# Optimization experiments

Measured on AMD Instinct MI355X. Metric: run time of the kernel, lower is better.

Reference implementation:

```python
import jax, jax.numpy as jnp
import numpy as np

MOVING_AVG_RATE = 0.999
EPS_NORM = 1e-12   # F.normalize eps
EPS_MEAN = 1e-6    # cluster mean denom eps


def _l2norm(a):
    n = jnp.linalg.norm(a, axis=1, keepdims=True)
    return a / jnp.maximum(n, EPS_NORM)


def setup_inputs() -> dict:
    key = jax.random.key(0)
    k1, k2 = jax.random.split(key)
    x = jax.random.normal(k1, (8, 512, 64, 64), dtype=jnp.float32)
    m = jax.random.normal(k2, (1024, 512), dtype=jnp.float32)  # codebook [k, c]
    return {"x": x, "m": m}


def reference(x, m):
    b, c, h, w = x.shape
    k = m.shape[0]
    # flatten spatial/batch dims -> tokens [N, c]
    xf = jnp.transpose(x, (0, 2, 3, 1)).reshape(-1, c)
    xn = _l2norm(xf)
    mn = _l2norm(m)
    score = xn @ mn.T  # [N, k] cosine similarity

    # EMA codebook update: hard assignment via argmax, scatter-reduce means
    idx = jnp.argmax(score, axis=1)  # [N]
    counts = jax.ops.segment_sum(jnp.ones(xf.shape[0], dtype=xf.dtype), idx, num_segments=k)
    esum = jax.ops.segment_sum(xf, idx, num_segments=k)  # [k, c]
    emean = esum / (counts[:, None] + EPS_MEAN)
    new_m = m * MOVING_AVG_RATE + emean * (1.0 - MOVING_AVG_RATE)

    # soft combine against the UPDATED codebook
    soft = jax.nn.softmax(score, axis=1)
    out = soft @ new_m  # [N, c]
    return jnp.transpose(out.reshape(b, h, w, c), (0, 3, 1, 2))
```

## Files before the change

### kernel.cpp

```cpp
#include <hip/hip_runtime.h>
#include <hip/hip_bf16.h>
#include <math.h>

#define B 8
#define C 512
#define H 64
#define W 64
#define N 32768
#define K 1024
#define HW 4096
#define CHW 2097152

typedef unsigned short u16;
typedef __attribute__((ext_vector_type(4))) float f32x4;
typedef __attribute__((ext_vector_type(8))) short bf16x8;

#define MNB_OFF   0
#define IDX_OFF   (MNB_OFF + K*C/2)
#define CNT_OFF   (IDX_OFF + N)
#define ESUM_OFF  (CNT_OFF + K)
#define NMT_OFF   (ESUM_OFF + K*C)
#define SCORE_OFF (NMT_OFF + K*C/2)

static __device__ __forceinline__ u16 f2bf(float f) {
    unsigned int u = __float_as_uint(f);
    u += 0x7fffu + ((u >> 16) & 1u);
    return (u16)(u >> 16);
}
static __device__ __forceinline__ float bf2f(unsigned int us) {
    return __uint_as_float(us << 16);
}
static __device__ __forceinline__ unsigned int pack2(float lo, float hi) {
    return (unsigned int)f2bf(lo) | ((unsigned int)f2bf(hi) << 16);
}

static __device__ __forceinline__ void gload_lds16(const void* g, void* l) {
    __builtin_amdgcn_global_load_lds(
        (const __attribute__((address_space(1))) unsigned int*)g,
        (__attribute__((address_space(3))) unsigned int*)l, 16, 0, 0);
}

__global__ void k_norm_mb(const float* __restrict__ m, u16* __restrict__ mnb) {
    int j = blockIdx.x;
    int lane = threadIdx.x;
    const float4* mr = (const float4*)(m + (size_t)j * C);
    float4 a = mr[lane * 2], b = mr[lane * 2 + 1];
    float ss = a.x*a.x + a.y*a.y + a.z*a.z + a.w*a.w
             + b.x*b.x + b.y*b.y + b.z*b.z + b.w*b.w;
#pragma unroll
    for (int o = 32; o >= 1; o >>= 1) ss += __shfl_xor(ss, o);
    float inv = 1.0f / fmaxf(sqrtf(ss), 1e-12f);
    uint4 pk;
    pk.x = pack2(a.x * inv, a.y * inv);
    pk.y = pack2(a.z * inv, a.w * inv);
    pk.z = pack2(b.x * inv, b.y * inv);
    pk.w = pack2(b.z * inv, b.w * inv);
    *(uint4*)(mnb + (size_t)j * C + lane * 8) = pk;
}

__global__ void __launch_bounds__(256) k_prep_x(const float* __restrict__ x,
                                                u16* __restrict__ xb) {
    int bh = blockIdx.x;
    int b = bh >> 6, h = bh & 63;
    int w  = threadIdx.x & 63;
    int wq = threadIdx.x >> 6;
    const float* base = x + (size_t)b * CHW + (size_t)h * W + w;
    float ss = 0.0f;
    for (int ch = wq * 128; ch < wq * 128 + 128; ++ch) {
        float v = base[(size_t)ch * HW];
        ss += v * v;
    }
    __shared__ float red[4][64];
    red[wq][w] = ss;
    __syncthreads();
    float tot = red[0][w] + red[1][w] + red[2][w] + red[3][w];
    float inv = 1.0f / fmaxf(sqrtf(tot), 1e-12f);
    size_t n = (size_t)bh * 64 + w;
    u16* orow = xb + n * C;
    for (int c8 = wq * 128; c8 < wq * 128 + 128; c8 += 8) {
        float v0 = base[(size_t)(c8+0)*HW] * inv;
        float v1 = base[(size_t)(c8+1)*HW] * inv;
        float v2 = base[(size_t)(c8+2)*HW] * inv;
        float v3 = base[(size_t)(c8+3)*HW] * inv;
        float v4 = base[(size_t)(c8+4)*HW] * inv;
        float v5 = base[(size_t)(c8+5)*HW] * inv;
        float v6 = base[(size_t)(c8+6)*HW] * inv;
        float v7 = base[(size_t)(c8+7)*HW] * inv;
        uint4 pk;
        pk.x = pack2(v0, v1); pk.y = pack2(v2, v3);
        pk.z = pack2(v4, v5); pk.w = pack2(v6, v7);
        *(uint4*)&orow[c8] = pk;
    }
}

__global__ void __launch_bounds__(256) k_score_mfma(
        const u16* __restrict__ xb, const u16* __restrict__ mnb,
        u16* __restrict__ score) {
    __shared__ u16 As[128 * 64];
    __shared__ u16 Bs[128 * 64];
    int tid = threadIdx.x;
    int lane = tid & 63;
    int wid = tid >> 6;
    int wm = wid >> 1, wn = wid & 1;
    int n0 = blockIdx.x * 128;
    int j0 = blockIdx.y * 128;

    f32x4 acc[4][4] = {};

    const u16* a_src = xb + (size_t)(n0 + wid*32 + (lane>>3)) * C + (lane&7)*8;
    const u16* b_src = mnb + (size_t)(j0 + wid*32 + (lane>>3)) * C + (lane&7)*8;

    for (int k0 = 0; k0 < C; k0 += 64) {
#pragma unroll
        for (int is = 0; is < 4; ++is) {
            gload_lds16(a_src + (size_t)is*8*C + k0, As + (wid*32 + is*8)*64);
            gload_lds16(b_src + (size_t)is*8*C + k0, Bs + (wid*32 + is*8)*64);
        }
        __syncthreads();
#pragma unroll
        for (int kh = 0; kh < 2; ++kh) {
            int kk = kh * 32;
            bf16x8 av[4], bv[4];
#pragma unroll
            for (int f = 0; f < 4; ++f) {
                av[f] = *(const bf16x8*)&As[(wm*64 + f*16 + (lane&15))*64 + kk + (lane>>4)*8];
                bv[f] = *(const bf16x8*)&Bs[(wn*64 + f*16 + (lane&15))*64 + kk + (lane>>4)*8];
            }
#pragma unroll
            for (int fm = 0; fm < 4; ++fm)
#pragma unroll
                for (int fn = 0; fn < 4; ++fn)
                    acc[fm][fn] = __builtin_amdgcn_mfma_f32_16x16x32_bf16(
                        av[fm], bv[fn], acc[fm][fn], 0, 0, 0);
        }
        __syncthreads();
    }
    int crow = (lane >> 4) * 4;
    int ccol = lane & 15;
#pragma unroll
    for (int fm = 0; fm < 4; ++fm) {
#pragma unroll
        for (int fn = 0; fn < 4; ++fn) {
            size_t rbase = (size_t)(n0 + wm*64 + fm*16 + crow) * K
                         + (j0 + wn*64 + fn*16 + ccol);
#pragma unroll
            for (int r = 0; r < 4; ++r)
                score[rbase + (size_t)r * K] = f2bf(acc[fm][fn][r]);
        }
    }
}

__global__ void k_rowstats(u16* __restrict__ score,
                           int* __restrict__ idx, float* __restrict__ counts) {
    int wq = threadIdx.x >> 6, lane = threadIdx.x & 63;
    int n = blockIdx.x * 4 + wq;
    u16* row = score + (size_t)n * K;
    uint4* rp = (uint4*)(row + lane * 16);
    uint4 q0 = rp[0], q1 = rp[1];
    float vals[16];
    unsigned int ws_[8] = {q0.x, q0.y, q0.z, q0.w, q1.x, q1.y, q1.z, q1.w};
#pragma unroll
    for (int e = 0; e < 8; ++e) {
        vals[2 * e]     = bf2f(ws_[e] & 0xffffu);
        vals[2 * e + 1] = bf2f(ws_[e] >> 16);
    }
    float best = -INFINITY; int bj = 0;
#pragma unroll
    for (int e = 0; e < 16; ++e) {
        if (vals[e] > best) { best = vals[e]; bj = lane * 16 + e; }
    }
#pragma unroll
    for (int o = 32; o >= 1; o >>= 1) {
        float ov = __shfl_xor(best, o);
        int   oj = __shfl_xor(bj, o);
        if (ov > best || (ov == best && oj < bj)) { best = ov; bj = oj; }
    }
    float p[16];
    float s = 0.0f;
#pragma unroll
    for (int e = 0; e < 16; ++e) { p[e] = __expf(vals[e] - best); s += p[e]; }
#pragma unroll
    for (int o = 32; o >= 1; o >>= 1) s += __shfl_xor(s, o);
    float sinv = 1.0f / s;
    uint4 o0, o1;
    o0.x = pack2(p[0]*sinv,  p[1]*sinv);
    o0.y = pack2(p[2]*sinv,  p[3]*sinv);
    o0.z = pack2(p[4]*sinv,  p[5]*sinv);
    o0.w = pack2(p[6]*sinv,  p[7]*sinv);
    o1.x = pack2(p[8]*sinv,  p[9]*sinv);
    o1.y = pack2(p[10]*sinv, p[11]*sinv);
    o1.z = pack2(p[12]*sinv, p[13]*sinv);
    o1.w = pack2(p[14]*sinv, p[15]*sinv);
    rp[0] = o0; rp[1] = o1;
    if (lane == 0) {
        idx[n] = bj;
        atomicAdd(&counts[bj], 1.0f);
    }
}

__global__ void __launch_bounds__(256) k_esum_ch(const float* __restrict__ x,
        const int* __restrict__ idx, float* __restrict__ esum) {
    int ch = blockIdx.x;
    __shared__ float part[K];
    for (int k = threadIdx.x; k < K; k += 256) part[k] = 0.0f;
    __syncthreads();
    const float* xc = x + (size_t)ch * HW;
    for (int t = threadIdx.x; t < N / 4; t += 256) {
        int n4 = t * 4;
        int b = n4 >> 12, hw = n4 & 4095;
        float4 v = *(const float4*)(xc + (size_t)b * CHW + hw);
        int4 id = *(const int4*)(idx + n4);
        atomicAdd(&part[id.x], v.x);
        atomicAdd(&part[id.y], v.y);
        atomicAdd(&part[id.z], v.z);
        atomicAdd(&part[id.w], v.w);
    }
    __syncthreads();
    for (int k = threadIdx.x; k < K; k += 256)
        esum[(size_t)k * C + ch] = part[k];
}

__global__ void __launch_bounds__(256) k_newm_t(const float* __restrict__ m,
        const float* __restrict__ esum, const float* __restrict__ counts,
        u16* __restrict__ nmt) {
    __shared__ float tile[64][65];
    int jb = blockIdx.x * 64, cb = blockIdx.y * 64;
    int cl = threadIdx.x & 63, jq = threadIdx.x >> 6;
#pragma unroll
    for (int r = 0; r < 16; ++r) {
        int jl = jq * 16 + r;
        int j = jb + jl;
        float sc = 0.001f / (counts[j] + 1e-6f);
        size_t off = (size_t)j * C + cb + cl;
        tile[jl][cl] = 0.999f * m[off] + esum[off] * sc;
    }
    __syncthreads();
    int crow = threadIdx.x >> 2;
    int q = threadIdx.x & 3;
    uint4 lo, hi;
    float v0  = tile[q*16+ 0][crow], v1  = tile[q*16+ 1][crow];
    float v2  = tile[q*16+ 2][crow], v3  = tile[q*16+ 3][crow];
    float v4  = tile[q*16+ 4][crow], v5  = tile[q*16+ 5][crow];
    float v6  = tile[q*16+ 6][crow], v7  = tile[q*16+ 7][crow];
    float v8  = tile[q*16+ 8][crow], v9  = tile[q*16+ 9][crow];
    float v10 = tile[q*16+10][crow], v11 = tile[q*16+11][crow];
    float v12 = tile[q*16+12][crow], v13 = tile[q*16+13][crow];
    float v14 = tile[q*16+14][crow], v15 = tile[q*16+15][crow];
    lo.x = pack2(v0, v1);  lo.y = pack2(v2, v3);
    lo.z = pack2(v4, v5);  lo.w = pack2(v6, v7);
    hi.x = pack2(v8, v9);  hi.y = pack2(v10, v11);
    hi.z = pack2(v12, v13); hi.w = pack2(v14, v15);
    u16* orow = nmt + (size_t)(cb + crow) * K + jb + q * 16;
    *(uint4*)orow = lo;
    *(uint4*)(orow + 8) = hi;
}

__global__ void __launch_bounds__(256) k_out_mfma(
        const u16* __restrict__ P, const u16* __restrict__ nmt,
        float* __restrict__ out) {
    __shared__ u16 As[128 * 64];
    __shared__ u16 Bs[128 * 64];
    int tid = threadIdx.x;
    int lane = tid & 63;
    int wid = tid >> 6;
    int wm = wid >> 1, wn = wid & 1;
    int n0 = blockIdx.x * 128;
    int c0 = blockIdx.y * 128;

    f32x4 acc[4][4] = {};

    const u16* a_src = P   + (size_t)(n0 + wid*32 + (lane>>3)) * K + (lane&7)*8;
    const u16* b_src = nmt + (size_t)(c0 + wid*32 + (lane>>3)) * K + (lane&7)*8;

    for (int k0 = 0; k0 < K; k0 += 64) {
#pragma unroll
        for (int is = 0; is < 4; ++is) {
            gload_lds16(a_src + (size_t)is*8*K + k0, As + (wid*32 + is*8)*64);
            gload_lds16(b_src + (size_t)is*8*K + k0, Bs + (wid*32 + is*8)*64);
        }
        __syncthreads();
#pragma unroll
        for (int kh = 0; kh < 2; ++kh) {
            int kk = kh * 32;
            bf16x8 av[4], bv[4];
#pragma unroll
            for (int f = 0; f < 4; ++f) {
                av[f] = *(const bf16x8*)&As[(wm*64 + f*16 + (lane&15))*64 + kk + (lane>>4)*8];
                bv[f] = *(const bf16x8*)&Bs[(wn*64 + f*16 + (lane&15))*64 + kk + (lane>>4)*8];
            }
#pragma unroll
            for (int fm = 0; fm < 4; ++fm)
#pragma unroll
                for (int fn = 0; fn < 4; ++fn)
                    acc[fm][fn] = __builtin_amdgcn_mfma_f32_16x16x32_bf16(
                        av[fm], bv[fn], acc[fm][fn], 0, 0, 0);
        }
        __syncthreads();
    }
    int b = n0 >> 12;
    int hw0 = (n0 & 4095) + wm * 64;
    int crow = (lane >> 4) * 4;
    int ccol = lane & 15;
    float* obase = out + (size_t)b * CHW;
#pragma unroll
    for (int fm = 0; fm < 4; ++fm) {
#pragma unroll
        for (int fn = 0; fn < 4; ++fn) {
            int ch = c0 + wn * 64 + fn * 16 + ccol;
            int hw = hw0 + fm * 16 + crow;
            float4 v = make_float4(acc[fm][fn][0], acc[fm][fn][1],
                                   acc[fm][fn][2], acc[fm][fn][3]);
            *(float4*)&obase[(size_t)ch * HW + hw] = v;
        }
    }
}

extern "C" void kernel_launch(void* const* d_in, const int* in_sizes, int n_in,
                              void* d_out, int out_size, void* d_ws, size_t ws_size,
                              hipStream_t stream) {
    const float* x = (const float*)d_in[0];
    const float* m = (const float*)d_in[1];
    float* out = (float*)d_out;
    float* ws = (float*)d_ws;

    u16*   mnb   = (u16*)(ws + MNB_OFF);
    int*   idx   = (int*)(ws + IDX_OFF);
    float* cnt   = ws + CNT_OFF;
    float* esum  = ws + ESUM_OFF;
    u16*   nmt   = (u16*)(ws + NMT_OFF);
    u16*   score = (u16*)(ws + SCORE_OFF);
    u16*   xb    = (u16*)d_out;

    hipMemsetAsync(cnt, 0, (size_t)K * sizeof(float), stream);

    k_norm_mb<<<K, 64, 0, stream>>>(m, mnb);
    k_prep_x<<<B * H, 256, 0, stream>>>(x, xb);
    k_score_mfma<<<dim3(N / 128, K / 128), 256, 0, stream>>>(xb, mnb, score);
    k_rowstats<<<N / 4, 256, 0, stream>>>(score, idx, cnt);
    k_esum_ch<<<C, 256, 0, stream>>>(x, idx, esum);
    k_newm_t<<<dim3(K / 64, C / 64), 256, 0, stream>>>(m, esum, cnt, nmt);
    k_out_mfma<<<dim3(N / 128, C / 128), 256, 0, stream>>>(score, nmt, out);
}
```

Baseline: 377.3 us.

## Split esum scatter across batch slices with partial buffers and a reduce pass

The per-channel esum kernel, which ran only 512 blocks each looping over all 32768 tokens, is split into 512x8 blocks that each handle one batch slice and write per-slice partial sums. A new reduce kernel adds the slices into a transposed [C,K] esum. The new-codebook kernel then reads this transposed layout with vector loads. This adds one kernel launch and a 16MB partial buffer, which lives in the output buffer as scratch space and is later overwritten by the final result.

```diff
diff --git a/kernel.cpp b/kernel.cpp
--- a/kernel.cpp
+++ b/kernel.cpp
@@ -10,6 +10,7 @@
 #define K 1024
 #define HW 4096
 #define CHW 2097152
+#define S 8
 
 typedef unsigned short u16;
 typedef __attribute__((ext_vector_type(4))) float f32x4;
@@ -18,9 +19,9 @@
 #define MNB_OFF   0
 #define IDX_OFF   (MNB_OFF + K*C/2)
 #define CNT_OFF   (IDX_OFF + N)
-#define ESUM_OFF  (CNT_OFF + K)
-#define NMT_OFF   (ESUM_OFF + K*C)
-#define SCORE_OFF (NMT_OFF + K*C/2)
+#define ESUMT_OFF (CNT_OFF + K)
+#define NMT_OFF   (ESUMT_OFF + C*K)
+#define SCORE_OFF (NMT_OFF + C*K/2)
 
 static __device__ __forceinline__ u16 f2bf(float f) {
     unsigned int u = __float_as_uint(f);
@@ -198,58 +199,76 @@
     }
 }
 
-__global__ void __launch_bounds__(256) k_esum_ch(const float* __restrict__ x,
-        const int* __restrict__ idx, float* __restrict__ esum) {
+__global__ void __launch_bounds__(256) k_esum_part(const float* __restrict__ x,
+        const int* __restrict__ idx, float* __restrict__ partial) {
     int ch = blockIdx.x;
+    int s  = blockIdx.y;
     __shared__ float part[K];
     for (int k = threadIdx.x; k < K; k += 256) part[k] = 0.0f;
     __syncthreads();
-    const float* xc = x + (size_t)ch * HW;
-    for (int t = threadIdx.x; t < N / 4; t += 256) {
-        int n4 = t * 4;
-        int b = n4 >> 12, hw = n4 & 4095;
-        float4 v = *(const float4*)(xc + (size_t)b * CHW + hw);
-        int4 id = *(const int4*)(idx + n4);
+    const float* xc = x + (size_t)s * CHW + (size_t)ch * HW;
+    const int*   ic = idx + s * HW;
+#pragma unroll
+    for (int it = 0; it < HW / 4 / 256; ++it) {
+        int t4 = (it * 256 + threadIdx.x) * 4;
+        float4 v = *(const float4*)(xc + t4);
+        int4 id = *(const int4*)(ic + t4);
         atomicAdd(&part[id.x], v.x);
         atomicAdd(&part[id.y], v.y);
         atomicAdd(&part[id.z], v.z);
         atomicAdd(&part[id.w], v.w);
     }
     __syncthreads();
-    for (int k = threadIdx.x; k < K; k += 256)
-        esum[(size_t)k * C + ch] = part[k];
+    float* prow = partial + ((size_t)s * C + ch) * K;
+    for (int k = threadIdx.x; k < K; k += 256) prow[k] = part[k];
+}
+
+__global__ void __launch_bounds__(256) k_esum_reduce(const float* __restrict__ partial,
+        float* __restrict__ esumT) {
+    int c = blockIdx.x;
+    int k4 = threadIdx.x * 4;
+    float4 acc = make_float4(0.f, 0.f, 0.f, 0.f);
+#pragma unroll
+    for (int s = 0; s < S; ++s) {
+        float4 v = *(const float4*)(partial + ((size_t)s * C + c) * K + k4);
+        acc.x += v.x; acc.y += v.y; acc.z += v.z; acc.w += v.w;
+    }
+    *(float4*)(esumT + (size_t)c * K + k4) = acc;
 }
 
 __global__ void __launch_bounds__(256) k_newm_t(const float* __restrict__ m,
-        const float* __restrict__ esum, const float* __restrict__ counts,
+        const float* __restrict__ esumT, const float* __restrict__ counts,
         u16* __restrict__ nmt) {
     __shared__ float tile[64][65];
+    __shared__ float scs[64];
     int jb = blockIdx.x * 64, cb = blockIdx.y * 64;
     int cl = threadIdx.x & 63, jq = threadIdx.x >> 6;
 #pragma unroll
     for (int r = 0; r < 16; ++r) {
         int jl = jq * 16 + r;
-        int j = jb + jl;
-        float sc = 0.001f / (counts[j] + 1e-6f);
-        size_t off = (size_t)j * C + cb + cl;
-        tile[jl][cl] = 0.999f * m[off] + esum[off] * sc;
-    }
+        tile[jl][cl] = m[(size_t)(jb + jl) * C + cb + cl];
+    }
+    if (threadIdx.x < 64)
+        scs[threadIdx.x] = 0.001f / (counts[jb + threadIdx.x] + 1e-6f);
     __syncthreads();
     int crow = threadIdx.x >> 2;
     int q = threadIdx.x & 3;
+    const float* erow = esumT + (size_t)(cb + crow) * K + jb + q * 16;
+    float4 e0 = *(const float4*)(erow + 0);
+    float4 e1 = *(const float4*)(erow + 4);
+    float4 e2 = *(const float4*)(erow + 8);
+    float4 e3 = *(const float4*)(erow + 12);
+    float ev[16] = {e0.x,e0.y,e0.z,e0.w, e1.x,e1.y,e1.z,e1.w,
+                    e2.x,e2.y,e2.z,e2.w, e3.x,e3.y,e3.z,e3.w};
+    float v[16];
+#pragma unroll
+    for (int t = 0; t < 16; ++t)
+        v[t] = 0.999f * tile[q*16 + t][crow] + ev[t] * scs[q*16 + t];
     uint4 lo, hi;
-    float v0  = tile[q*16+ 0][crow], v1  = tile[q*16+ 1][crow];
-    float v2  = tile[q*16+ 2][crow], v3  = tile[q*16+ 3][crow];
-    float v4  = tile[q*16+ 4][crow], v5  = tile[q*16+ 5][crow];
-    float v6  = tile[q*16+ 6][crow], v7  = tile[q*16+ 7][crow];
-    float v8  = tile[q*16+ 8][crow], v9  = tile[q*16+ 9][crow];
-    float v10 = tile[q*16+10][crow], v11 = tile[q*16+11][crow];
-    float v12 = tile[q*16+12][crow], v13 = tile[q*16+13][crow];
-    float v14 = tile[q*16+14][crow], v15 = tile[q*16+15][crow];
-    lo.x = pack2(v0, v1);  lo.y = pack2(v2, v3);
-    lo.z = pack2(v4, v5);  lo.w = pack2(v6, v7);
-    hi.x = pack2(v8, v9);  hi.y = pack2(v10, v11);
-    hi.z = pack2(v12, v13); hi.w = pack2(v14, v15);
+    lo.x = pack2(v[0], v[1]);   lo.y = pack2(v[2], v[3]);
+    lo.z = pack2(v[4], v[5]);   lo.w = pack2(v[6], v[7]);
+    hi.x = pack2(v[8], v[9]);   hi.y = pack2(v[10], v[11]);
+    hi.z = pack2(v[12], v[13]); hi.w = pack2(v[14], v[15]);
     u16* orow = nmt + (size_t)(cb + crow) * K + jb + q * 16;
     *(uint4*)orow = lo;
     *(uint4*)(orow + 8) = hi;
@@ -326,10 +345,11 @@
     u16*   mnb   = (u16*)(ws + MNB_OFF);
     int*   idx   = (int*)(ws + IDX_OFF);
     float* cnt   = ws + CNT_OFF;
-    float* esum  = ws + ESUM_OFF;
+    float* esumT = ws + ESUMT_OFF;
     u16*   nmt   = (u16*)(ws + NMT_OFF);
     u16*   score = (u16*)(ws + SCORE_OFF);
-    u16*   xb    = (u16*)d_out;
+    u16*   xb      = (u16*)d_out;
+    float* partial = (float*)((char*)d_out + (size_t)32 * 1024 * 1024);
 
     hipMemsetAsync(cnt, 0, (size_t)K * sizeof(float), stream);
 
@@ -337,7 +357,8 @@
     k_prep_x<<<B * H, 256, 0, stream>>>(x, xb);
     k_score_mfma<<<dim3(N / 128, K / 128), 256, 0, stream>>>(xb, mnb, score);
     k_rowstats<<<N / 4, 256, 0, stream>>>(score, idx, cnt);
-    k_esum_ch<<<C, 256, 0, stream>>>(x, idx, esum);
-    k_newm_t<<<dim3(K / 64, C / 64), 256, 0, stream>>>(m, esum, cnt, nmt);
+    k_esum_part<<<dim3(C, S), 256, 0, stream>>>(x, idx, partial);
+    k_esum_reduce<<<C, 256, 0, stream>>>(partial, esumT);
+    k_newm_t<<<dim3(K / 64, C / 64), 256, 0, stream>>>(m, esumT, cnt, nmt);
     k_out_mfma<<<dim3(N / 128, C / 128), 256, 0, stream>>>(score, nmt, out);
 }
```

Result: no change. 382.8 us (+1.5%).
